# Optimization experiments

Measured on AMD Instinct MI355X. Metric: run time of the kernel, lower is better.

The kernel has to match this reference:

```python
import jax, jax.numpy as jnp
import numpy as np

B, T, D = 4, 4096, 1024


def setup_inputs() -> dict:
    key = jax.random.key(0)
    ks = jax.random.split(key, 10)
    scale = 1.0 / np.sqrt(D)
    x = jax.random.normal(ks[0], (B, T, D), jnp.float32)
    last_x = jnp.zeros((D,), jnp.float32)
    last_num = jnp.zeros((D,), jnp.float32)
    last_den = jnp.zeros((D,), jnp.float32)
    time_decay = jax.random.normal(ks[1], (D,), jnp.float32) * 0.1
    time_first = jax.random.normal(ks[2], (D,), jnp.float32) * 0.1
    time_mix_k = jax.random.uniform(ks[3], (1, 1, D), jnp.float32)
    time_mix_v = jax.random.uniform(ks[4], (1, 1, D), jnp.float32)
    time_mix_r = jax.random.uniform(ks[5], (1, 1, D), jnp.float32)
    Wk = jax.random.normal(ks[6], (D, D), jnp.float32) * scale
    Wv = jax.random.normal(ks[7], (D, D), jnp.float32) * scale
    Wr = jax.random.normal(ks[8], (D, D), jnp.float32) * scale
    Wo = jax.random.normal(ks[9], (D, D), jnp.float32) * scale
    return {"x": x, "last_x": last_x, "last_num": last_num, "last_den": last_den,
            "time_decay": time_decay, "time_first": time_first,
            "time_mix_k": time_mix_k, "time_mix_v": time_mix_v, "time_mix_r": time_mix_r,
            "Wk": Wk, "Wv": Wv, "Wr": Wr, "Wo": Wo}


def reference(x, last_x, last_num, last_den, time_decay, time_first,
              time_mix_k, time_mix_v, time_mix_r, Wk, Wv, Wr, Wo):
    # token-shift lerps against the incoming state (broadcast over B, T)
    k = jnp.einsum('btd,ed->bte', x * time_mix_k + last_x * (1.0 - time_mix_k), Wk)
    v = jnp.einsum('btd,ed->bte', x * time_mix_v + last_x * (1.0 - time_mix_v), Wv)
    r = jnp.einsum('btd,ed->bte', x * time_mix_r + last_x * (1.0 - time_mix_r), Wr)
    # WKV numerics, exactly as the original (no extra stabilization)
    efk = jnp.exp(time_first + k)          # exp(time_first + k), [B,T,D]
    wkv = (last_num + efk * v) / (last_den + efk)
    rwkv = jax.nn.sigmoid(r) * wkv
    decay = jnp.exp(-jnp.exp(time_decay))  # [D]
    ek = jnp.exp(k)
    num = decay * last_num + ek * v
    den = decay * last_den + ek
    out = jnp.einsum('btd,ed->bte', rwkv, Wo)
    return out, x[..., -1, :], num[..., -1, :], den[..., -1, :]
```

## Files before the change

### kernel.cpp

```cpp
#include <hip/hip_runtime.h>
#include <cstdint>
#include <cstddef>

constexpr int DD = 1024;
constexpr int TT = 4096;
constexpr int BB = 4;
constexpr int MM = BB * TT;

typedef __bf16 bf16x8 __attribute__((ext_vector_type(8)));
typedef float  f32x4  __attribute__((ext_vector_type(4)));

__device__ __forceinline__ unsigned short f2bf(float f) {
  union { float f; uint32_t u; } c; c.f = f;
  uint32_t r = (c.u + 0x7FFFu + ((c.u >> 16) & 1u)) >> 16;
  return (unsigned short)r;
}

__device__ __forceinline__ float fast_rcp(float x) {
  return __builtin_amdgcn_rcpf(x);
}

__device__ __forceinline__ void async_ld16(const unsigned short* g, unsigned short* lds_dst) {
  __builtin_amdgcn_global_load_lds(
      (const __attribute__((address_space(1))) void*)g,
      (__attribute__((address_space(3))) void*)lds_dst,
      16, 0, 0);
}

#define VWAIT(n) asm volatile("s_waitcnt vmcnt(" #n ")" ::: "memory")

__global__ void prep_all(const float* __restrict__ Wk, const float* __restrict__ Wv,
                         const float* __restrict__ Wr, const float* __restrict__ Wo,
                         const float* __restrict__ tmk, const float* __restrict__ tmv,
                         const float* __restrict__ tmr,
                         const float* __restrict__ last_x,
                         const float4* __restrict__ x,
                         unsigned short* __restrict__ wz,
                         unsigned short* __restrict__ wo,
                         float* __restrict__ bias,
                         ushort4* __restrict__ xb,
                         float4* __restrict__ out_xlast) {
  if (blockIdx.x < 1024) {
    int w = (blockIdx.x * 256 + threadIdx.x) >> 6;
    int lane = threadIdx.x & 63;
    int z = w >> 10;
    int e = w & (DD - 1);
    const float* W  = (z == 0) ? Wk  : (z == 1) ? Wv  : (z == 2) ? Wr : Wo;
    const float* tm = (z == 0) ? tmk : (z == 1) ? tmv : tmr;
    unsigned short* dst = (z < 3) ? (wz + (size_t)z * DD * DD + (size_t)e * DD)
                                  : (wo + (size_t)e * DD);
    float s = 0.f;
#pragma unroll
    for (int j = 0; j < 4; ++j) {
      int d = j * 256 + lane * 4;
      float4 wv4 = *(const float4*)(W + (size_t)e * DD + d);
      if (z < 3) {
        float4 t4 = *(const float4*)(tm + d);
        float4 l4 = *(const float4*)(last_x + d);
        s += l4.x * (1.f - t4.x) * wv4.x + l4.y * (1.f - t4.y) * wv4.y +
             l4.z * (1.f - t4.z) * wv4.z + l4.w * (1.f - t4.w) * wv4.w;
        wv4.x *= t4.x; wv4.y *= t4.y; wv4.z *= t4.z; wv4.w *= t4.w;
      }
      ushort4 o;
      o.x = f2bf(wv4.x); o.y = f2bf(wv4.y); o.z = f2bf(wv4.z); o.w = f2bf(wv4.w);
      *(ushort4*)(dst + d) = o;
    }
    if (z < 3) {
      for (int off = 32; off; off >>= 1) s += __shfl_down(s, off, 64);
      if (lane == 0) bias[z * DD + e] = s;
    }
  } else {
    int i = (blockIdx.x - 1024) * 256 + threadIdx.x;
    float4 v = x[i];
    ushort4 o;
    o.x = f2bf(v.x); o.y = f2bf(v.y); o.z = f2bf(v.z); o.w = f2bf(v.w);
    xb[i] = o;
    int m = i >> 8;
    if ((m & (TT - 1)) == (TT - 1)) {
      int b = m >> 12;
      out_xlast[b * 256 + (i & 255)] = v;
    }
  }
}

__global__ __launch_bounds__(512, 2) void gemm_kvr(
    const unsigned short* __restrict__ A,
    const unsigned short* __restrict__ Wz,
    const float* __restrict__ bias,
    const float* __restrict__ time_first, const float* __restrict__ time_decay,
    const float* __restrict__ last_num, const float* __restrict__ last_den,
    unsigned short* __restrict__ rwkv,
    float* __restrict__ out_num, float* __restrict__ out_den) {
  __shared__ __align__(1024) unsigned short rA[4][256 * 32];
  __shared__ __align__(1024) unsigned short rB[4][192 * 32];
  const int tid  = threadIdx.x;
  const int lane = tid & 63;
  const int wave = tid >> 6;

  const int id  = blockIdx.y * gridDim.x + blockIdx.x;
  const int xcd = id & 7;
  const int s_  = id >> 3;
  const int m0 = (xcd * 8 + (s_ >> 4)) * 256;
  const int n0 = (s_ & 15) * 64;

  const int wm = (wave >> 1) * 64;
  const int wn = (wave & 1) * 32;
  const int fr = lane & 15;
  const int fq = lane >> 4;

  int phA[4], phB[3][2];
#pragma unroll
  for (int m = 0; m < 4; ++m) {
    int row = wm + m * 16 + fr;
    phA[m] = row * 64 + ((fq ^ (row & 3) ^ ((row >> 2) & 3)) << 4);
  }
#pragma unroll
  for (int z = 0; z < 3; ++z)
#pragma unroll
    for (int n = 0; n < 2; ++n) {
      int row = z * 64 + wn + n * 16 + fr;
      phB[z][n] = row * 64 + ((fq ^ (row & 3) ^ ((row >> 2) & 3)) << 4);
    }

  const int g_log = (lane & 3) ^ ((lane >> 2) & 3) ^ ((lane >> 4) & 3);
  size_t srcOff[4];
  int dstOff[4];
  if (wave < 4) {
#pragma unroll
    for (int j = 0; j < 4; ++j) {
      int idx = wave * 4 + j;
      int r = idx * 16 + (lane >> 2);
      srcOff[j] = (size_t)(m0 + r) * DD + g_log * 8;
      dstOff[j] = idx * 1024;
    }
  } else {
#pragma unroll
    for (int j = 0; j < 3; ++j) {
      int idx = (wave - 4) * 3 + j;
      int r = idx * 16 + (lane >> 2);
      int z = r >> 6, zr = r & 63;
      srcOff[j] = (size_t)z * DD * DD + (size_t)(n0 + zr) * DD + g_log * 8;
      dstOff[j] = idx * 1024;
    }
  }

  auto stage = [&](int slot, int stp) {
    const int ke = stp * 32;
    if (wave < 4) {
#pragma unroll
      for (int j = 0; j < 4; ++j)
        async_ld16(A + srcOff[j] + ke, (unsigned short*)((char*)rA[slot] + dstOff[j]));
    } else {
#pragma unroll
      for (int j = 0; j < 3; ++j)
        async_ld16(Wz + srcOff[j] + ke, (unsigned short*)((char*)rB[slot] + dstOff[j]));
    }
  };

  f32x4 acc[3][4][2] = {};

  stage(0, 0);
  stage(1, 1);
  stage(2, 2);
  if (wave < 4) VWAIT(8); else VWAIT(6);
  __builtin_amdgcn_sched_barrier(0);
  __builtin_amdgcn_s_barrier();
  __builtin_amdgcn_sched_barrier(0);

#pragma unroll 1
  for (int s = 0; s < 32; ++s) {
    const int slot = s & 3;
    bf16x8 af[4];
#pragma unroll
    for (int m = 0; m < 4; ++m)
      af[m] = *(const bf16x8*)((const char*)rA[slot] + phA[m]);
    bf16x8 bfr[3][2];
#pragma unroll
    for (int z = 0; z < 3; ++z)
#pragma unroll
      for (int n = 0; n < 2; ++n)
        bfr[z][n] = *(const bf16x8*)((const char*)rB[slot] + phB[z][n]);

    if (s < 29) stage((s + 3) & 3, s + 3);

    __builtin_amdgcn_s_barrier();
    asm volatile("s_waitcnt lgkmcnt(0)" ::: "memory");
    __builtin_amdgcn_sched_barrier(0);
    __builtin_amdgcn_s_setprio(1);
#pragma unroll
    for (int z = 0; z < 3; ++z)
#pragma unroll
      for (int m = 0; m < 4; ++m)
#pragma unroll
        for (int n = 0; n < 2; ++n)
          acc[z][m][n] = __builtin_amdgcn_mfma_f32_16x16x32_bf16(
              af[m], bfr[z][n], acc[z][m][n], 0, 0, 0);
    __builtin_amdgcn_s_setprio(0);

    if (s < 31) {
      if (s < 29)       { if (wave < 4) VWAIT(8); else VWAIT(6); }
      else if (s == 29) { if (wave < 4) VWAIT(4); else VWAIT(3); }
      else              { VWAIT(0); }
      __builtin_amdgcn_sched_barrier(0);
      __builtin_amdgcn_s_barrier();
      __builtin_amdgcn_sched_barrier(0);
    }
  }

  const int crow = fq * 4;
  const int ccol = fr;
#pragma unroll
  for (int ni = 0; ni < 2; ++ni) {
    int gnz = n0 + wn + ni * 16 + ccol;
    float bk = bias[gnz], bv = bias[DD + gnz], br = bias[2 * DD + gnz];
    float tf = time_first[gnz];
    float ln = last_num[gnz], ld = last_den[gnz];
    float dec = __expf(-__expf(time_decay[gnz]));
#pragma unroll
    for (int mi = 0; mi < 4; ++mi) {
#pragma unroll
      for (int r = 0; r < 4; ++r) {
        int gm = m0 + wm + mi * 16 + crow + r;
        float kk = acc[0][mi][ni][r] + bk;
        float vv = acc[1][mi][ni][r] + bv;
        float rr = acc[2][mi][ni][r] + br;
        float efk = __expf(tf + kk);
        float wkv = (ln + efk * vv) * fast_rcp(ld + efk);
        float sr  = fast_rcp(1.0f + __expf(-rr));
        rwkv[(size_t)gm * DD + gnz] = f2bf(sr * wkv);
        if ((gm & (TT - 1)) == (TT - 1)) {
          int b = gm >> 12;
          float ek = __expf(kk);
          out_num[b * DD + gnz] = dec * ln + ek * vv;
          out_den[b * DD + gnz] = dec * ld + ek;
        }
      }
    }
  }
}

__global__ void gemm_bt128(const unsigned short* __restrict__ A,
                           const unsigned short* __restrict__ Bw,
                           float* __restrict__ Cf,
                           int M, int N, int K) {
  __shared__ unsigned short lA[2][128 * 32];
  __shared__ unsigned short lB[2][128 * 32];
  const int tid  = threadIdx.x;
  const int lane = tid & 63;
  const int wave = tid >> 6;

  const int nBlocks = N >> 7;
  const int mBlocks = M >> 7;
  const int id  = blockIdx.y * gridDim.x + blockIdx.x;
  const int xcd = id & 7;
  const int s   = id >> 3;
  const int mPer = mBlocks >> 3;
  const int m0 = (xcd * mPer + s / nBlocks) * 128;
  const int n0 = (s % nBlocks) * 128;

  const int wm = (wave >> 1) * 64;
  const int wn = (wave & 1) * 64;

  f32x4 acc[4][4] = {};
  const int fr_row = lane & 15;
  const int fr_kb  = (lane >> 4) * 16;
  const int scol = (tid & 3) * 8;

  for (int k0 = 0; k0 < K; k0 += 64) {
    __syncthreads();
#pragma unroll
    for (int h = 0; h < 2; ++h) {
      int kk = k0 + h * 32;
#pragma unroll
      for (int it = 0; it < 2; ++it) {
        int cc  = it * 256 + tid;
        int row = cc >> 2;
        async_ld16(A + (size_t)(m0 + row) * K + (kk + scol),
                   lA[h] + (size_t)(it * 256 + wave * 64) * 8);
      }
#pragma unroll
      for (int it = 0; it < 2; ++it) {
        int cc  = it * 256 + tid;
        int row = cc >> 2;
        async_ld16(Bw + (size_t)(n0 + row) * K + (kk + scol),
                   lB[h] + (size_t)(it * 256 + wave * 64) * 8);
      }
    }
    __syncthreads();

#pragma unroll
    for (int h = 0; h < 2; ++h) {
      bf16x8 af[4], bfr[4];
#pragma unroll
      for (int i = 0; i < 4; ++i) {
        af[i]  = *(const bf16x8*)((const char*)lA[h] + ((wm + i * 16 + fr_row) * 64 + fr_kb));
        bfr[i] = *(const bf16x8*)((const char*)lB[h] + ((wn + i * 16 + fr_row) * 64 + fr_kb));
      }
#pragma unroll
      for (int mi = 0; mi < 4; ++mi)
#pragma unroll
        for (int ni = 0; ni < 4; ++ni)
          acc[mi][ni] = __builtin_amdgcn_mfma_f32_16x16x32_bf16(af[mi], bfr[ni], acc[mi][ni], 0, 0, 0);
    }
  }

  const int crow = (lane >> 4) * 4;
  const int ccol = lane & 15;
#pragma unroll
  for (int mi = 0; mi < 4; ++mi) {
#pragma unroll
    for (int ni = 0; ni < 4; ++ni) {
      int gn = n0 + wn + ni * 16 + ccol;
#pragma unroll
      for (int r = 0; r < 4; ++r) {
        int gm = m0 + wm + mi * 16 + crow + r;
        Cf[(size_t)gm * N + gn] = acc[mi][ni][r];
      }
    }
  }
}

extern "C" void kernel_launch(void* const* d_in, const int* in_sizes, int n_in,
                              void* d_out, int out_size, void* d_ws, size_t ws_size,
                              hipStream_t stream) {
  const float* x          = (const float*)d_in[0];
  const float* last_x     = (const float*)d_in[1];
  const float* last_num   = (const float*)d_in[2];
  const float* last_den   = (const float*)d_in[3];
  const float* time_decay = (const float*)d_in[4];
  const float* time_first = (const float*)d_in[5];
  const float* tmk        = (const float*)d_in[6];
  const float* tmv        = (const float*)d_in[7];
  const float* tmr        = (const float*)d_in[8];
  const float* Wk         = (const float*)d_in[9];
  const float* Wv         = (const float*)d_in[10];
  const float* Wr         = (const float*)d_in[11];
  const float* Wo         = (const float*)d_in[12];

  float* out       = (float*)d_out;
  float* out_xlast = out + (size_t)MM * DD;
  float* out_num   = out_xlast + BB * DD;
  float* out_den   = out_num + BB * DD;

  char* ws = (char*)d_ws;
  unsigned short* xb   = (unsigned short*)ws;
  unsigned short* wz   = (unsigned short*)(ws + 33554432);
  unsigned short* wo   = (unsigned short*)(ws + 39845888);
  float*          bias = (float*)(ws + 41943040);
  unsigned short* rwkv = (unsigned short*)(ws + 41955328);

  prep_all<<<1024 + MM * DD / 4 / 256, 256, 0, stream>>>(
      Wk, Wv, Wr, Wo, tmk, tmv, tmr, last_x, (const float4*)x,
      wz, wo, bias, (ushort4*)xb, (float4*)out_xlast);

  gemm_kvr<<<dim3(16, 64), 512, 0, stream>>>(
      xb, wz, bias, time_first, time_decay, last_num, last_den,
      rwkv, out_num, out_den);

  gemm_bt128<<<dim3(DD / 128, MM / 128), 256, 0, stream>>>(
      rwkv, wo, out, MM, DD, DD);
}
```

Baseline: 335.3 us.

## Interleave LDS fragment reads with MFMA groups and simplify LDS swizzle

```diff
diff --git a/kernel.cpp b/kernel.cpp
--- a/kernel.cpp
+++ b/kernel.cpp
@@ -28,6 +28,10 @@
 }
 
 #define VWAIT(n) asm volatile("s_waitcnt vmcnt(" #n ")" ::: "memory")
+#define LWAIT(n) asm volatile("s_waitcnt lgkmcnt(" #n ")" ::: "memory")
+#define SB()     __builtin_amdgcn_sched_barrier(0)
+
+__device__ __forceinline__ int swzb(int b) { return b ^ (((b >> 9) & 1) << 5); }
 
 __global__ void prep_all(const float* __restrict__ Wk, const float* __restrict__ Wv,
                          const float* __restrict__ Wr, const float* __restrict__ Wo,
@@ -110,36 +114,35 @@
 
   int phA[4], phB[3][2];
 #pragma unroll
-  for (int m = 0; m < 4; ++m) {
-    int row = wm + m * 16 + fr;
-    phA[m] = row * 64 + ((fq ^ (row & 3) ^ ((row >> 2) & 3)) << 4);
-  }
+  for (int m = 0; m < 4; ++m)
+    phA[m] = swzb((wm + m * 16 + fr) * 64 + fq * 16);
 #pragma unroll
   for (int z = 0; z < 3; ++z)
 #pragma unroll
-    for (int n = 0; n < 2; ++n) {
-      int row = z * 64 + wn + n * 16 + fr;
-      phB[z][n] = row * 64 + ((fq ^ (row & 3) ^ ((row >> 2) & 3)) << 4);
-    }
-
-  const int g_log = (lane & 3) ^ ((lane >> 2) & 3) ^ ((lane >> 4) & 3);
+    for (int n = 0; n < 2; ++n)
+      phB[z][n] = swzb((z * 64 + wn + n * 16 + fr) * 64 + fq * 16);
+
   size_t srcOff[4];
   int dstOff[4];
   if (wave < 4) {
 #pragma unroll
     for (int j = 0; j < 4; ++j) {
       int idx = wave * 4 + j;
-      int r = idx * 16 + (lane >> 2);
-      srcOff[j] = (size_t)(m0 + r) * DD + g_log * 8;
+      int pb = idx * 1024 + lane * 16;
+      int lq = swzb(pb);
+      int r = lq >> 6, cb = lq & 63;
+      srcOff[j] = (size_t)(m0 + r) * DD + cb / 2;
       dstOff[j] = idx * 1024;
     }
   } else {
 #pragma unroll
     for (int j = 0; j < 3; ++j) {
       int idx = (wave - 4) * 3 + j;
-      int r = idx * 16 + (lane >> 2);
+      int pb = idx * 1024 + lane * 16;
+      int lq = swzb(pb);
+      int r = lq >> 6, cb = lq & 63;
       int z = r >> 6, zr = r & 63;
-      srcOff[j] = (size_t)z * DD * DD + (size_t)(n0 + zr) * DD + g_log * 8;
+      srcOff[j] = (size_t)z * DD * DD + (size_t)(n0 + zr) * DD + cb / 2;
       dstOff[j] = idx * 1024;
     }
   }
@@ -163,47 +166,69 @@
   stage(1, 1);
   stage(2, 2);
   if (wave < 4) VWAIT(8); else VWAIT(6);
-  __builtin_amdgcn_sched_barrier(0);
+  SB();
   __builtin_amdgcn_s_barrier();
-  __builtin_amdgcn_sched_barrier(0);
 
 #pragma unroll 1
   for (int s = 0; s < 32; ++s) {
     const int slot = s & 3;
+    if (s < 29) stage((s + 3) & 3, s + 3);
+
     bf16x8 af[4];
 #pragma unroll
     for (int m = 0; m < 4; ++m)
       af[m] = *(const bf16x8*)((const char*)rA[slot] + phA[m]);
-    bf16x8 bfr[3][2];
-#pragma unroll
-    for (int z = 0; z < 3; ++z)
+    bf16x8 b0[2];
+#pragma unroll
+    for (int n = 0; n < 2; ++n)
+      b0[n] = *(const bf16x8*)((const char*)rB[slot] + phB[0][n]);
+    SB();
+    bf16x8 b1[2];
+#pragma unroll
+    for (int n = 0; n < 2; ++n)
+      b1[n] = *(const bf16x8*)((const char*)rB[slot] + phB[1][n]);
+    SB();
+    bf16x8 b2[2];
+#pragma unroll
+    for (int n = 0; n < 2; ++n)
+      b2[n] = *(const bf16x8*)((const char*)rB[slot] + phB[2][n]);
+    SB();
+
+    LWAIT(4); SB();
+    __builtin_amdgcn_s_setprio(1);
+#pragma unroll
+    for (int m = 0; m < 4; ++m)
 #pragma unroll
       for (int n = 0; n < 2; ++n)
-        bfr[z][n] = *(const bf16x8*)((const char*)rB[slot] + phB[z][n]);
-
-    if (s < 29) stage((s + 3) & 3, s + 3);
-
-    __builtin_amdgcn_s_barrier();
-    asm volatile("s_waitcnt lgkmcnt(0)" ::: "memory");
-    __builtin_amdgcn_sched_barrier(0);
+        acc[0][m][n] = __builtin_amdgcn_mfma_f32_16x16x32_bf16(
+            af[m], b0[n], acc[0][m][n], 0, 0, 0);
+    __builtin_amdgcn_s_setprio(0);
+
+    LWAIT(2); SB();
     __builtin_amdgcn_s_setprio(1);
 #pragma unroll
-    for (int z = 0; z < 3; ++z)
-#pragma unroll
-      for (int m = 0; m < 4; ++m)
-#pragma unroll
-        for (int n = 0; n < 2; ++n)
-          acc[z][m][n] = __builtin_amdgcn_mfma_f32_16x16x32_bf16(
-              af[m], bfr[z][n], acc[z][m][n], 0, 0, 0);
+    for (int m = 0; m < 4; ++m)
+#pragma unroll
+      for (int n = 0; n < 2; ++n)
+        acc[1][m][n] = __builtin_amdgcn_mfma_f32_16x16x32_bf16(
+            af[m], b1[n], acc[1][m][n], 0, 0, 0);
+    __builtin_amdgcn_s_setprio(0);
+
+    LWAIT(0); SB();
+    __builtin_amdgcn_s_setprio(1);
+#pragma unroll
+    for (int m = 0; m < 4; ++m)
+#pragma unroll
+      for (int n = 0; n < 2; ++n)
+        acc[2][m][n] = __builtin_amdgcn_mfma_f32_16x16x32_bf16(
+            af[m], b2[n], acc[2][m][n], 0, 0, 0);
     __builtin_amdgcn_s_setprio(0);
 
     if (s < 31) {
       if (s < 29)       { if (wave < 4) VWAIT(8); else VWAIT(6); }
       else if (s == 29) { if (wave < 4) VWAIT(4); else VWAIT(3); }
       else              { VWAIT(0); }
-      __builtin_amdgcn_sched_barrier(0);
       __builtin_amdgcn_s_barrier();
-      __builtin_amdgcn_sched_barrier(0);
     }
   }
 
```

After: 346.6 us. 1.03x slower.
